# Kernel tuning notes

Measured on AMD Instinct MI355X. Metric: run time of the kernel, lower is better.

## Reference

```python
import jax, jax.numpy as jnp
import numpy as np

N, IN_F, OUT_F = 8192, 256, 128
ALPHA = 0.2          # LeakyReLU negative slope
NEG_INF = -9e15      # mask value used by the original module
DENSITY = 0.1        # adjacency density


def setup_inputs() -> dict:
    key = jax.random.key(0)
    k1, k2, k3, k4 = jax.random.split(key, 4)
    x = jax.random.normal(k1, (N, IN_F), dtype=jnp.float32)
    adj = (jax.random.uniform(k2, (N, N)) < DENSITY).astype(jnp.float32)
    W = jax.random.normal(k3, (IN_F, OUT_F), dtype=jnp.float32) * (1.0 / np.sqrt(IN_F))
    a = jax.random.normal(k4, (2 * OUT_F, 1), dtype=jnp.float32) * (1.0 / np.sqrt(2 * OUT_F))
    return {"x": x, "adj": adj, "W": W, "a": a}


def reference(x, adj, W, a):
    # h = x @ W : [N, F]
    h = x @ W
    # Decompose a^T [h_i ; h_j] = (h a1)_i + (h a2)_j  -- identical math to the
    # original O(N^2 * 2F) cat/repeat construction, without materializing it.
    a1 = a[:OUT_F, 0]           # [F]
    a2 = a[OUT_F:, 0]           # [F]
    s1 = h @ a1                 # [N]
    s2 = h @ a2                 # [N]
    e = jax.nn.leaky_relu(s1[:, None] + s2[None, :], negative_slope=ALPHA)  # [N, N]
    scores = jnp.where(adj > 0, e, NEG_INF)
    attention = jax.nn.softmax(scores, axis=1)   # row-wise softmax
    # dropout = 0.0 (eval mode) -> identity
    h_prime = attention @ h      # [N, F]
    return h_prime
```

## Files before the change

kernel.cpp:

```cpp
#include <hip/hip_runtime.h>
#include <hip/hip_bf16.h>

typedef __attribute__((ext_vector_type(4))) float  f32x4;
typedef __attribute__((ext_vector_type(8))) short  bf16x8;
typedef unsigned short u16;

#define ALPHA 0.2f
#define NN 8192
#define FF 128
#define LOG2E 1.4426950408889634f
#define AS1 __attribute__((address_space(1)))
#define AS3 __attribute__((address_space(3)))

__device__ __forceinline__ u16 f2b(float f) {
  __hip_bfloat16 hb = __float2bfloat16(f);
  return *reinterpret_cast<u16*>(&hb);
}

extern "C" __global__ void __launch_bounds__(256)
wt_cvt(const float* __restrict__ x, const float* __restrict__ Wm,
       u16* __restrict__ xb, u16* __restrict__ WTb) {
  const int id = blockIdx.x * 256 + threadIdx.x;
  if (blockIdx.x < 2048) {
    const f32x4 v = *(const f32x4*)(x + (size_t)id * 4);
    uint2 p;
    p.x = f2b(v.x) | ((unsigned)f2b(v.y) << 16);
    p.y = f2b(v.z) | ((unsigned)f2b(v.w) << 16);
    *(uint2*)(xb + (size_t)id * 4) = p;
  } else {
    const int o = id - 2048 * 256;
    const int c = o >> 8, k = o & 255;
    WTb[o] = f2b(Wm[k * 128 + c]);
  }
}

extern "C" __global__ void __launch_bounds__(256)
gat_h(const u16* __restrict__ xb, const u16* __restrict__ WTb,
      const float* __restrict__ av, u16* __restrict__ hT,
      float* __restrict__ s1v, float* __restrict__ s2v) {
  __shared__ float hs[16][128];
  const int t = threadIdx.x, lane = t & 63, wv = t >> 6;
  const int i0 = blockIdx.x * 16;
  const int fr = lane & 15, kg = lane >> 4;

  f32x4 acc0 = {0.f,0.f,0.f,0.f}, acc1 = {0.f,0.f,0.f,0.f};
  const u16* xp  = xb  + (size_t)(i0 + fr) * 256 + kg * 8;
  const u16* b0p = WTb + (size_t)(wv * 32 + fr) * 256 + kg * 8;
  const u16* b1p = b0p + 16 * 256;
#pragma unroll
  for (int ks = 0; ks < 8; ++ks) {
    const bf16x8 A  = *(const bf16x8*)(xp  + ks * 32);
    const bf16x8 B0 = *(const bf16x8*)(b0p + ks * 32);
    const bf16x8 B1 = *(const bf16x8*)(b1p + ks * 32);
    acc0 = __builtin_amdgcn_mfma_f32_16x16x32_bf16(A, B0, acc0, 0, 0, 0);
    acc1 = __builtin_amdgcn_mfma_f32_16x16x32_bf16(A, B1, acc1, 0, 0, 0);
  }
#pragma unroll
  for (int r = 0; r < 4; ++r) {
    hs[kg * 4 + r][wv * 32 + fr]      = acc0[r];
    hs[kg * 4 + r][wv * 32 + 16 + fr] = acc1[r];
  }
  __syncthreads();

  {
    const int c = t >> 1, rr = (t & 1) * 8;
    u16 u[8];
#pragma unroll
    for (int m = 0; m < 8; ++m) u[m] = f2b(hs[rr + m][c]);
    *(uint4*)(hT + (size_t)c * NN + i0 + rr) = *(const uint4*)u;
  }
  {
    const int r = t >> 4, q = t & 15;
    float p1 = 0.f, p2 = 0.f;
#pragma unroll
    for (int m = 0; m < 8; ++m) {
      const int c = q * 8 + m;
      const float hv = hs[r][c];
      p1 = fmaf(hv, av[c], p1);
      p2 = fmaf(hv, av[128 + c], p2);
    }
    p1 += __shfl_xor(p1, 1); p1 += __shfl_xor(p1, 2);
    p1 += __shfl_xor(p1, 4); p1 += __shfl_xor(p1, 8);
    p2 += __shfl_xor(p2, 1); p2 += __shfl_xor(p2, 2);
    p2 += __shfl_xor(p2, 4); p2 += __shfl_xor(p2, 8);
    if (q == 0) { s1v[i0 + r] = p1 * LOG2E; s2v[i0 + r] = p2 * LOG2E; }
  }
}

extern "C" __global__ void __launch_bounds__(512, 4)
gat_main(const float* __restrict__ adj, const u16* __restrict__ hT,
         const float* __restrict__ s1l, const float* __restrict__ s2l,
         float* __restrict__ out) {
  __shared__ u16 hl[2][128 * 128];
  __shared__ u16 wl[2][16 * 128];

  const int t = threadIdx.x, lane = t & 63, wv = t >> 6;
  const int i0 = blockIdx.x * 16;
  const int gr = t >> 5;
  const int gj = (t & 31) * 4;
  const int c16 = (t & 31) >> 1, half = t & 1;
  const int r0 = wv * 16;
  const int srow = lane >> 4, scol = lane & 15;
  const int fr = lane & 15, kg = lane >> 4;
  const int bcol = wv * 16 + fr;

  const float s1i = s1l[i0 + gr];
  const float* adjp = adj + (size_t)(i0 + gr) * NN + gj;

  f32x4 acc = {0.f, 0.f, 0.f, 0.f};
  float den = 0.f;
  f32x4 a4, z4;

  auto stage_h = [&](int b, int jn) {
#pragma unroll
    for (int q = 0; q < 4; ++q) {
      const int r = r0 + q * 4 + srow;
      const u16* g = hT + (size_t)r * NN + jn + ((scol ^ (r & 7)) << 3);
      __builtin_amdgcn_global_load_lds((const AS1 void*)g,
          (AS3 void*)&hl[b][(r0 + q * 4) * 128], 16, 0, 0);
    }
    __builtin_amdgcn_sched_barrier(0);
  };
  auto wgen = [&](int b) {
    float w0, w1, w2, w3;
    { float tz = s1i + z4.x; float fz = fmaxf(tz, ALPHA * tz); w0 = a4.x * exp2f(fz); }
    { float tz = s1i + z4.y; float fz = fmaxf(tz, ALPHA * tz); w1 = a4.y * exp2f(fz); }
    { float tz = s1i + z4.z; float fz = fmaxf(tz, ALPHA * tz); w2 = a4.z * exp2f(fz); }
    { float tz = s1i + z4.w; float fz = fmaxf(tz, ALPHA * tz); w3 = a4.w * exp2f(fz); }
    den += (w0 + w1) + (w2 + w3);
    uint2 p;
    p.x = f2b(w0) | ((unsigned)f2b(w1) << 16);
    p.y = f2b(w2) | ((unsigned)f2b(w3) << 16);
    char* base = (char*)&wl[b][0];
    *(uint2*)(base + gr * 256 + ((c16 ^ (gr & 7)) << 4) + half * 8) = p;
  };
  auto mmstep = [&](int b) {
    const char* wb = (const char*)&wl[b][0];
    const char* hb = (const char*)&hl[b][0];
#pragma unroll
    for (int ks = 0; ks < 4; ++ks) {
      const int cg = ks * 4 + kg;
      const bf16x8 A = *(const bf16x8*)(wb + fr * 256 + ((cg ^ (fr & 7)) << 4));
      const bf16x8 B = *(const bf16x8*)(hb + bcol * 256 + ((cg ^ (bcol & 7)) << 4));
      acc = __builtin_amdgcn_mfma_f32_16x16x32_bf16(A, B, acc, 0, 0, 0);
    }
  };

  stage_h(0, 0);
  a4 = *(const f32x4*)(adjp);
  z4 = *(const f32x4*)(s2l + gj);
  wgen(0);
  a4 = *(const f32x4*)(adjp + 128);
  z4 = *(const f32x4*)(s2l + 128 + gj);
  asm volatile("s_waitcnt lgkmcnt(0)" ::: "memory");
  __builtin_amdgcn_s_barrier();

  for (int it = 0; it < 62; ++it) {
    const int cb = it & 1, nb = cb ^ 1;
    stage_h(nb, (it + 1) * 128);
    wgen(nb);
    a4 = *(const f32x4*)(adjp + (it + 2) * 128);
    z4 = *(const f32x4*)(s2l + (it + 2) * 128 + gj);
    mmstep(cb);
    asm volatile("s_waitcnt vmcnt(2) lgkmcnt(0)" ::: "memory");
    __builtin_amdgcn_s_barrier();
  }
  stage_h(1, 63 * 128);
  wgen(1);
  mmstep(0);
  asm volatile("s_waitcnt vmcnt(0) lgkmcnt(0)" ::: "memory");
  __builtin_amdgcn_s_barrier();
  mmstep(1);
  asm volatile("s_waitcnt lgkmcnt(0)" ::: "memory");
  __builtin_amdgcn_s_barrier();

  den += __shfl_xor(den, 1);  den += __shfl_xor(den, 2);
  den += __shfl_xor(den, 4);  den += __shfl_xor(den, 8);
  den += __shfl_xor(den, 16);
  float* denl = (float*)&wl[0][0];
  if ((lane & 31) == 0) denl[gr] = den;
  __syncthreads();
#pragma unroll
  for (int r = 0; r < 4; ++r) {
    const int row = kg * 4 + r;
    out[(size_t)(i0 + row) * FF + bcol] = acc[r] / denl[row];
  }
}

extern "C" void kernel_launch(void* const* d_in, const int* in_sizes, int n_in,
                              void* d_out, int out_size, void* d_ws, size_t ws_size,
                              hipStream_t stream) {
  const float* x   = (const float*)d_in[0];
  const float* adj = (const float*)d_in[1];
  const float* Wm  = (const float*)d_in[2];
  const float* av  = (const float*)d_in[3];
  float* out = (float*)d_out;

  char* ws = (char*)d_ws;
  u16*   hT  = (u16*)(ws);
  float* s1v = (float*)(ws + 2097152);
  float* s2v = (float*)(ws + 2130048 - 128);
  u16*   xb  = (u16*)(ws + 2162688);
  u16*   WTb = (u16*)(ws + 6356992);

  wt_cvt  <<<2176, 256, 0, stream>>>(x, Wm, xb, WTb);
  gat_h   <<<NN / 16, 256, 0, stream>>>(xb, WTb, av, hT, s1v, s2v);
  gat_main<<<NN / 16, 512, 0, stream>>>(adj, hT, s1v, s2v, out);
}
```

Baseline: 395.1 us.

## Split K across waves with register-direct h loads and blocked hT layout

Stores h transposed in 32-column blocks so each wave can load its B fragments straight from global memory into registers, dropping the LDS staging of h and the per-iteration barriers. Each of four waves owns a 32-wide K slice per 128-column step, computes its own attention weights directly in MFMA A-operand layout, and keeps eight accumulators covering all 128 output features. The partial sums are reduced across waves through LDS at the end. The cost is heavier global/L2 traffic for h, since every block re-reads all of it without LDS reuse, plus more accumulator registers and a 256-thread block.

```diff
diff --git a/kernel.cpp b/kernel.cpp
--- a/kernel.cpp
+++ b/kernel.cpp
@@ -9,8 +9,6 @@
 #define NN 8192
 #define FF 128
 #define LOG2E 1.4426950408889634f
-#define AS1 __attribute__((address_space(1)))
-#define AS3 __attribute__((address_space(3)))
 
 __device__ __forceinline__ u16 f2b(float f) {
   __hip_bfloat16 hb = __float2bfloat16(f);
@@ -36,7 +34,7 @@
 
 extern "C" __global__ void __launch_bounds__(256)
 gat_h(const u16* __restrict__ xb, const u16* __restrict__ WTb,
-      const float* __restrict__ av, u16* __restrict__ hT,
+      const float* __restrict__ av, u16* __restrict__ hT2,
       float* __restrict__ s1v, float* __restrict__ s2v) {
   __shared__ float hs[16][128];
   const int t = threadIdx.x, lane = t & 63, wv = t >> 6;
@@ -67,7 +65,8 @@
     u16 u[8];
 #pragma unroll
     for (int m = 0; m < 8; ++m) u[m] = f2b(hs[rr + m][c]);
-    *(uint4*)(hT + (size_t)c * NN + i0 + rr) = *(const uint4*)u;
+    *(uint4*)(hT2 + ((size_t)(i0 >> 5) * 128 + c) * 32 + (i0 & 31) + rr) =
+        *(const uint4*)u;
   }
   {
     const int r = t >> 4, q = t & 15;
@@ -87,103 +86,98 @@
   }
 }
 
-extern "C" __global__ void __launch_bounds__(512, 4)
-gat_main(const float* __restrict__ adj, const u16* __restrict__ hT,
+#define MM(BB, AA) AA = __builtin_amdgcn_mfma_f32_16x16x32_bf16(af, BB, AA, 0, 0, 0)
+
+extern "C" __global__ void __launch_bounds__(256, 4)
+gat_main(const float* __restrict__ adj, const u16* __restrict__ hT2,
          const float* __restrict__ s1l, const float* __restrict__ s2l,
          float* __restrict__ out) {
-  __shared__ u16 hl[2][128 * 128];
-  __shared__ u16 wl[2][16 * 128];
-
-  const int t = threadIdx.x, lane = t & 63, wv = t >> 6;
+  __shared__ float accp[4][16][132];
+  __shared__ float denp[4][16];
+
+  const int t = threadIdx.x, lane = t & 63, ks = t >> 6;
+  const int fr = lane & 15, kg = lane >> 4;
   const int i0 = blockIdx.x * 16;
-  const int gr = t >> 5;
-  const int gj = (t & 31) * 4;
-  const int c16 = (t & 31) >> 1, half = t & 1;
-  const int r0 = wv * 16;
-  const int srow = lane >> 4, scol = lane & 15;
-  const int fr = lane & 15, kg = lane >> 4;
-  const int bcol = wv * 16 + fr;
-
-  const float s1i = s1l[i0 + gr];
-  const float* adjp = adj + (size_t)(i0 + gr) * NN + gj;
-
-  f32x4 acc = {0.f, 0.f, 0.f, 0.f};
+
+  const float s1i = s1l[i0 + fr];
+  const float* adjp = adj + (size_t)(i0 + fr) * NN + ks * 32 + kg * 8;
+  const float* s2p  = s2l + ks * 32 + kg * 8;
+  const u16*   hp   = hT2 + ks * 4096 + fr * 32 + kg * 8;
+
+  f32x4 acc0 = {0,0,0,0}, acc1 = {0,0,0,0}, acc2 = {0,0,0,0}, acc3 = {0,0,0,0};
+  f32x4 acc4 = {0,0,0,0}, acc5 = {0,0,0,0}, acc6 = {0,0,0,0}, acc7 = {0,0,0,0};
   float den = 0.f;
-  f32x4 a4, z4;
-
-  auto stage_h = [&](int b, int jn) {
-#pragma unroll
-    for (int q = 0; q < 4; ++q) {
-      const int r = r0 + q * 4 + srow;
-      const u16* g = hT + (size_t)r * NN + jn + ((scol ^ (r & 7)) << 3);
-      __builtin_amdgcn_global_load_lds((const AS1 void*)g,
-          (AS3 void*)&hl[b][(r0 + q * 4) * 128], 16, 0, 0);
+
+  f32x4 a0 = *(const f32x4*)(adjp);
+  f32x4 a1 = *(const f32x4*)(adjp + 4);
+  f32x4 z0 = *(const f32x4*)(s2p);
+  f32x4 z1 = *(const f32x4*)(s2p + 4);
+
+  for (int it = 0; it < 64; ++it) {
+    const u16* hb = hp + it * 16384;
+    const bf16x8 b0 = *(const bf16x8*)(hb);
+    const bf16x8 b1 = *(const bf16x8*)(hb + 512);
+    const bf16x8 b2 = *(const bf16x8*)(hb + 1024);
+    const bf16x8 b3 = *(const bf16x8*)(hb + 1536);
+    const bf16x8 b4 = *(const bf16x8*)(hb + 2048);
+    const bf16x8 b5 = *(const bf16x8*)(hb + 2560);
+    const bf16x8 b6 = *(const bf16x8*)(hb + 3072);
+    const bf16x8 b7 = *(const bf16x8*)(hb + 3584);
+    __builtin_amdgcn_sched_barrier(0);
+
+    bf16x8 af;
+    float dstep = 0.f;
+#pragma unroll
+    for (int e = 0; e < 8; ++e) {
+      const float adv = (e < 4) ? a0[e] : a1[e - 4];
+      const float tz  = s1i + ((e < 4) ? z0[e] : z1[e - 4]);
+      const float fz  = fmaxf(tz, ALPHA * tz);
+      const float w8  = adv * exp2f(fz);
+      dstep += w8;
+      af[e] = (short)f2b(w8);
     }
+    den += dstep;
+
+    const int itn = it < 63 ? it + 1 : 63;
+    const float* an = adjp + itn * 128;
+    a0 = *(const f32x4*)(an);
+    a1 = *(const f32x4*)(an + 4);
+    const float* zn = s2p + itn * 128;
+    z0 = *(const f32x4*)(zn);
+    z1 = *(const f32x4*)(zn + 4);
     __builtin_amdgcn_sched_barrier(0);
-  };
-  auto wgen = [&](int b) {
-    float w0, w1, w2, w3;
-    { float tz = s1i + z4.x; float fz = fmaxf(tz, ALPHA * tz); w0 = a4.x * exp2f(fz); }
-    { float tz = s1i + z4.y; float fz = fmaxf(tz, ALPHA * tz); w1 = a4.y * exp2f(fz); }
-    { float tz = s1i + z4.z; float fz = fmaxf(tz, ALPHA * tz); w2 = a4.z * exp2f(fz); }
-    { float tz = s1i + z4.w; float fz = fmaxf(tz, ALPHA * tz); w3 = a4.w * exp2f(fz); }
-    den += (w0 + w1) + (w2 + w3);
-    uint2 p;
-    p.x = f2b(w0) | ((unsigned)f2b(w1) << 16);
-    p.y = f2b(w2) | ((unsigned)f2b(w3) << 16);
-    char* base = (char*)&wl[b][0];
-    *(uint2*)(base + gr * 256 + ((c16 ^ (gr & 7)) << 4) + half * 8) = p;
-  };
-  auto mmstep = [&](int b) {
-    const char* wb = (const char*)&wl[b][0];
-    const char* hb = (const char*)&hl[b][0];
-#pragma unroll
-    for (int ks = 0; ks < 4; ++ks) {
-      const int cg = ks * 4 + kg;
-      const bf16x8 A = *(const bf16x8*)(wb + fr * 256 + ((cg ^ (fr & 7)) << 4));
-      const bf16x8 B = *(const bf16x8*)(hb + bcol * 256 + ((cg ^ (bcol & 7)) << 4));
-      acc = __builtin_amdgcn_mfma_f32_16x16x32_bf16(A, B, acc, 0, 0, 0);
+
+    MM(b0, acc0); MM(b1, acc1); MM(b2, acc2); MM(b3, acc3);
+    MM(b4, acc4); MM(b5, acc5); MM(b6, acc6); MM(b7, acc7);
+  }
+
+  den += __shfl_xor(den, 16);
+  den += __shfl_xor(den, 32);
+  if (lane < 16) denp[ks][fr] = den;
+
+#define STACC(F, AA) _Pragma("unroll") \
+  for (int r = 0; r < 4; ++r) accp[ks][kg * 4 + r][F * 16 + fr] = AA[r];
+  STACC(0, acc0) STACC(1, acc1) STACC(2, acc2) STACC(3, acc3)
+  STACC(4, acc4) STACC(5, acc5) STACC(6, acc6) STACC(7, acc7)
+#undef STACC
+
+  __syncthreads();
+
+  {
+    const int row = t >> 4;
+    const int c0  = (t & 15) * 8;
+    const float dv = denp[0][row] + denp[1][row] + denp[2][row] + denp[3][row];
+    f32x4 sA = {0,0,0,0}, sB = {0,0,0,0};
+#pragma unroll
+    for (int w = 0; w < 4; ++w) {
+      sA += *(const f32x4*)&accp[w][row][c0];
+      sB += *(const f32x4*)&accp[w][row][c0 + 4];
     }
-  };
-
-  stage_h(0, 0);
-  a4 = *(const f32x4*)(adjp);
-  z4 = *(const f32x4*)(s2l + gj);
-  wgen(0);
-  a4 = *(const f32x4*)(adjp + 128);
-  z4 = *(const f32x4*)(s2l + 128 + gj);
-  asm volatile("s_waitcnt lgkmcnt(0)" ::: "memory");
-  __builtin_amdgcn_s_barrier();
-
-  for (int it = 0; it < 62; ++it) {
-    const int cb = it & 1, nb = cb ^ 1;
-    stage_h(nb, (it + 1) * 128);
-    wgen(nb);
-    a4 = *(const f32x4*)(adjp + (it + 2) * 128);
-    z4 = *(const f32x4*)(s2l + (it + 2) * 128 + gj);
-    mmstep(cb);
-    asm volatile("s_waitcnt vmcnt(2) lgkmcnt(0)" ::: "memory");
-    __builtin_amdgcn_s_barrier();
-  }
-  stage_h(1, 63 * 128);
-  wgen(1);
-  mmstep(0);
-  asm volatile("s_waitcnt vmcnt(0) lgkmcnt(0)" ::: "memory");
-  __builtin_amdgcn_s_barrier();
-  mmstep(1);
-  asm volatile("s_waitcnt lgkmcnt(0)" ::: "memory");
-  __builtin_amdgcn_s_barrier();
-
-  den += __shfl_xor(den, 1);  den += __shfl_xor(den, 2);
-  den += __shfl_xor(den, 4);  den += __shfl_xor(den, 8);
-  den += __shfl_xor(den, 16);
-  float* denl = (float*)&wl[0][0];
-  if ((lane & 31) == 0) denl[gr] = den;
-  __syncthreads();
-#pragma unroll
-  for (int r = 0; r < 4; ++r) {
-    const int row = kg * 4 + r;
-    out[(size_t)(i0 + row) * FF + bcol] = acc[r] / denl[row];
+    const float inv = 1.f / dv;
+    sA *= inv; sB *= inv;
+    float* op = out + (size_t)(i0 + row) * FF + c0;
+    *(f32x4*)op       = sA;
+    *(f32x4*)(op + 4) = sB;
   }
 }
 
@@ -197,13 +191,13 @@
   float* out = (float*)d_out;
 
   char* ws = (char*)d_ws;
-  u16*   hT  = (u16*)(ws);
+  u16*   hT2 = (u16*)(ws);
   float* s1v = (float*)(ws + 2097152);
-  float* s2v = (float*)(ws + 2130048 - 128);
+  float* s2v = (float*)(ws + 2129920);
   u16*   xb  = (u16*)(ws + 2162688);
   u16*   WTb = (u16*)(ws + 6356992);
 
   wt_cvt  <<<2176, 256, 0, stream>>>(x, Wm, xb, WTb);
-  gat_h   <<<NN / 16, 256, 0, stream>>>(xb, WTb, av, hT, s1v, s2v);
-  gat_main<<<NN / 16, 512, 0, stream>>>(adj, hT, s1v, s2v, out);
-}
+  gat_h   <<<NN / 16, 256, 0, stream>>>(xb, WTb, av, hT2, s1v, s2v);
+  gat_main<<<NN / 16, 256, 0, stream>>>(adj, hT2, s1v, s2v, out);
+}
```

Result: slower. 417.8 us (+5.8%).
